# Kernel tuning notes

Measured on AMD Instinct MI355X. Metric: run time of the kernel, lower is better.

Reference implementation:

```python
import jax, jax.numpy as jnp
import numpy as np
from jax import lax

NUM_GROUPS = 16
EPS = 1e-5  # PyTorch GroupNorm default
POOL = 2
CLAMP_MIN, CLAMP_MAX = 0.0, 1.0


def setup_inputs() -> dict:
    key = jax.random.key(0)
    ks = jax.random.split(key, 6)
    B, Cin, H, W = 32, 64, 128, 128
    Cout, K = 128, 3
    return {
        "x": jax.random.normal(ks[0], (B, Cin, H, W), dtype=jnp.float32),
        "conv_w": jax.random.normal(ks[1], (Cout, Cin, K, K), dtype=jnp.float32),
        "conv_b": jax.random.normal(ks[2], (Cout,), dtype=jnp.float32),
        "gn_w": jax.random.normal(ks[3], (Cout,), dtype=jnp.float32),
        "gn_b": jax.random.normal(ks[4], (Cout,), dtype=jnp.float32),
        "scale": jax.random.normal(ks[5], (Cout, 1, 1), dtype=jnp.float32),
    }


def reference(x, conv_w, conv_b, gn_w, gn_b, scale):
    # Conv2d, stride 1, no padding (PyTorch default): [B,Cout,H-2,W-2]
    y = lax.conv_general_dilated(
        x, conv_w, window_strides=(1, 1), padding="VALID",
        dimension_numbers=("NCHW", "OIHW", "NCHW"))
    y = y + conv_b[None, :, None, None]

    # GroupNorm over (C/G, H, W) per sample and group
    B, C, H, W = y.shape
    yg = y.reshape(B, NUM_GROUPS, C // NUM_GROUPS, H, W)
    mean = jnp.mean(yg, axis=(2, 3, 4), keepdims=True)
    var = jnp.var(yg, axis=(2, 3, 4), keepdims=True)
    yn = ((yg - mean) * lax.rsqrt(var + EPS)).reshape(B, C, H, W)
    yn = yn * gn_w[None, :, None, None] + gn_b[None, :, None, None]

    # channel-wise scale (scale shape [C,1,1])
    yn = yn * scale[None, :, :, :]

    # MaxPool2d(kernel=2, stride=2)
    p = lax.reduce_window(yn, -jnp.inf, lax.max,
                          (1, 1, POOL, POOL), (1, 1, POOL, POOL), "VALID")

    # clamp
    return jnp.clip(p, CLAMP_MIN, CLAMP_MAX)
```

## Files before the change

### kernel.cpp

```cpp
#include <hip/hip_runtime.h>
#include <hip/hip_fp16.h>

#define CIN   64
#define COUT  128
#define HIN   128
#define WIN   128
#define HOUT  126
#define WOUT  126
#define HP    63
#define WP    63
#define NB    32
#define NG    16
#define EPS   1e-5f
#define KTOT  576
#define NTILE 252

#define XTROW (WIN * 64)
#define XTIMG (HIN * XTROW)

#define LROW  2176
#define LROWB 4352

typedef __attribute__((ext_vector_type(8))) _Float16 half8;
typedef __attribute__((ext_vector_type(4))) float f32x4;

#define GLOAD_LDS(gsrc, ldst)                                              \
    __builtin_amdgcn_global_load_lds(                                      \
        (const __attribute__((address_space(1))) void*)(gsrc),             \
        (__attribute__((address_space(3))) void*)(ldst), 16, 0, 0)

__global__ __launch_bounds__(256) void wprep_kernel(
    const float* __restrict__ cw, ushort* __restrict__ wt)
{
    int idx = blockIdx.x * 256 + threadIdx.x;
    if (idx >= COUT * KTOT) return;
    int co = idx / KTOT, k = idx - co * KTOT;
    int khw = k >> 6, ci = k & 63;
    float v = cw[(co * CIN + ci) * 9 + khw];
    wt[idx] = __half_as_ushort(__float2half(v));
}

__global__ __launch_bounds__(512) void xprep_kernel(
    const float* __restrict__ x, ushort* __restrict__ xt)
{
    const int tid = threadIdx.x;
    const int row = blockIdx.x & 127, b = blockIdx.x >> 7;
    const int cig = tid >> 6;
    const float* xb = x + (size_t)b * (CIN * HIN * WIN) + (size_t)row * WIN;
    ushort* ob = xt + (size_t)b * XTIMG + (size_t)row * XTROW;
#pragma unroll
    for (int ch = 0; ch < 2; ++ch) {
        int col = ch * 64 + (tid & 63);
        ushort v[8];
#pragma unroll
        for (int j = 0; j < 8; ++j)
            v[j] = __half_as_ushort(__float2half(
                xb[(size_t)(cig * 8 + j) * (HIN * WIN) + col]));
        uint4 pk;
        pk.x = (unsigned)v[0] | ((unsigned)v[1] << 16);
        pk.y = (unsigned)v[2] | ((unsigned)v[3] << 16);
        pk.z = (unsigned)v[4] | ((unsigned)v[5] << 16);
        pk.w = (unsigned)v[6] | ((unsigned)v[7] << 16);
        *(uint4*)(ob + col * 64 + ((cig ^ (col & 7)) * 8)) = pk;
    }
}

__global__ __launch_bounds__(256, 4) void conv_mfma_kernel(
    const ushort* __restrict__ xt, const ushort* __restrict__ wt,
    const float* __restrict__ cb, const float* __restrict__ gwv,
    const float* __restrict__ scv, float* __restrict__ m,
    float* __restrict__ partials)
{
    __shared__ ushort xs[4 * LROW];

    const int tid = threadIdx.x;
    const int bid = blockIdx.x;
    const int w   = (bid & 7) * 1008 + (bid >> 3);
    const int b   = w / 252;
    const int r   = w - b * 252;
    const int rp  = r >> 2;
    const int ct  = r & 3;
    const int r0x = rp * 2;

    const int l = tid & 63, wg = tid >> 6;
    const int l15 = l & 15, lhi = l >> 4;

    const ushort* xtb = xt + (size_t)b * XTIMG + (size_t)r0x * XTROW
                      + (size_t)(ct * 32) * 64;
#pragma unroll
    for (int t = 0; t < 5; ++t) {
        int idx = t * 256 + tid;
        if (idx < 1088) {
            int row = idx / 272;
            int within = idx - row * 272;
            GLOAD_LDS(xtb + (size_t)row * XTROW + within * 8, &xs[idx * 8]);
        }
    }
    __syncthreads();

    f32x4 acc[2][4];
#pragma unroll
    for (int mt = 0; mt < 2; ++mt)
#pragma unroll
        for (int nt = 0; nt < 4; ++nt)
            acc[mt][nt] = (f32x4){0.f, 0.f, 0.f, 0.f};

    const ushort* wb = wt + (size_t)(wg * 32 + l15) * KTOT + lhi * 8;
    const char* xsb = (const char*)xs;

#pragma unroll
    for (int khw = 0; khw < 9; ++khw) {
        const int kh = khw / 3, kw = khw - kh * 3;
        const int c7 = (l15 + kw) & 7;
#pragma unroll
        for (int cip = 0; cip < 2; ++cip) {
            half8 a0 = *(const half8*)(wb + khw * 64 + cip * 32);
            half8 a1 = *(const half8*)(wb + 16 * KTOT + khw * 64 + cip * 32);
            const int s = ((cip * 4 + lhi) ^ c7) * 16;
            half8 bv[4];
#pragma unroll
            for (int nt = 0; nt < 4; ++nt)
                bv[nt] = *(const half8*)(xsb + ((nt >> 1) + kh) * LROWB
                        + ((nt & 1) * 16 + kw + l15) * 128 + s);
#pragma unroll
            for (int nt = 0; nt < 4; ++nt) {
                acc[0][nt] = __builtin_amdgcn_mfma_f32_16x16x32_f16(
                    a0, bv[nt], acc[0][nt], 0, 0, 0);
                acc[1][nt] = __builtin_amdgcn_mfma_f32_16x16x32_f16(
                    a1, bv[nt], acc[1][nt], 0, 0, 0);
            }
        }
    }

#pragma unroll
    for (int mt = 0; mt < 2; ++mt) {
        float s1 = 0.f, s2 = 0.f;
#pragma unroll
        for (int r2 = 0; r2 < 4; ++r2) {
            int co = wg * 32 + mt * 16 + lhi * 4 + r2;
            float bias = cb[co];
            bool usemax = (gwv[co] * scv[co]) >= 0.f;
#pragma unroll
            for (int nc = 0; nc < 2; ++nc) {
                float v0 = acc[mt][nc][r2] + bias;
                float v1 = acc[mt][2 + nc][r2] + bias;
                int col = ct * 32 + nc * 16 + l15;
                if (col < WOUT) { s1 += v0 + v1; s2 += v0 * v0 + v1 * v1; }
                float a = usemax ? fmaxf(v0, v1) : fminf(v0, v1);
                float xo = __shfl_xor(a, 1);
                float wv = usemax ? fmaxf(a, xo) : fminf(a, xo);
                int wp = col >> 1;
                if (((l15 & 1) == 0) && wp < WP)
                    m[(((size_t)(b * COUT + co)) * HP + rp) * WP + wp] = wv;
            }
        }
#pragma unroll
        for (int d = 1; d < 16; d <<= 1) {
            s1 += __shfl_xor(s1, d);
            s2 += __shfl_xor(s2, d);
        }
        s1 += __shfl_xor(s1, 16);
        s2 += __shfl_xor(s2, 16);
        if (l15 == 0 && (lhi & 1) == 0) {
            int g = wg * 4 + mt * 2 + (lhi >> 1);
            size_t pidx = (((size_t)b * NG + g) * NTILE + (rp * 4 + ct)) * 2;
            partials[pidx + 0] = s1;
            partials[pidx + 1] = s2;
        }
    }
}

__global__ __launch_bounds__(64) void stats_kernel(
    const float* __restrict__ partials, float* __restrict__ stats)
{
    int t = blockIdx.x;
    int lane = threadIdx.x;
    float s1 = 0.f, s2 = 0.f;
    for (int j = lane; j < NTILE; j += 64) {
        s1 += partials[((size_t)t * NTILE + j) * 2 + 0];
        s2 += partials[((size_t)t * NTILE + j) * 2 + 1];
    }
#pragma unroll
    for (int d = 1; d < 64; d <<= 1) {
        s1 += __shfl_xor(s1, d);
        s2 += __shfl_xor(s2, d);
    }
    if (lane == 0) {
        const float N = 8.f * HOUT * WOUT;
        float mean = s1 / N;
        float var = s2 / N - mean * mean;
        stats[t * 2 + 0] = mean;
        stats[t * 2 + 1] = rsqrtf(var + EPS);
    }
}

__global__ __launch_bounds__(256) void final_kernel(
    const f32x4* __restrict__ m4, const float* __restrict__ stats,
    const float* __restrict__ gw, const float* __restrict__ gb,
    const float* __restrict__ sc, f32x4* __restrict__ out4)
{
    int idx = blockIdx.x * 256 + threadIdx.x;
    if (idx >= (NB * COUT * HP * WP) / 4) return;
    f32x4 v = m4[idx];
    f32x4 o;
    const int e0 = idx * 4;
#pragma unroll
    for (int j = 0; j < 4; ++j) {
        int e = e0 + j;
        int plane = e / (HP * WP);
        int c = plane & 127;
        int b = plane >> 7;
        int g = c >> 3;
        float mean = stats[(b * NG + g) * 2 + 0];
        float rstd = stats[(b * NG + g) * 2 + 1];
        float ga = rstd * gw[c] * sc[c];
        float gbb = (gb[c] - mean * rstd * gw[c]) * sc[c];
        o[j] = fminf(fmaxf(fmaf(v[j], ga, gbb), 0.f), 1.f);
    }
    out4[idx] = o;
}

extern "C" void kernel_launch(void* const* d_in, const int* in_sizes, int n_in,
                              void* d_out, int out_size, void* d_ws, size_t ws_size,
                              hipStream_t stream)
{
    const float* x  = (const float*)d_in[0];
    const float* cw = (const float*)d_in[1];
    const float* cbias = (const float*)d_in[2];
    const float* gw = (const float*)d_in[3];
    const float* gb = (const float*)d_in[4];
    const float* sc = (const float*)d_in[5];

    const size_t MSZ = (size_t)NB * COUT * HP * WP;
    float* m        = (float*)d_ws;
    float* partials = m + MSZ;
    float* stats    = partials + (size_t)NB * NG * NTILE * 2;
    ushort* wt      = (ushort*)(stats + 1024);
    ushort* xtb     = wt + (size_t)COUT * KTOT;

    hipLaunchKernelGGL(wprep_kernel, dim3((COUT * KTOT + 255) / 256), dim3(256),
                       0, stream, cw, wt);

    hipLaunchKernelGGL(xprep_kernel, dim3(NB * HIN), dim3(512), 0, stream,
                       x, xtb);

    hipLaunchKernelGGL(conv_mfma_kernel, dim3(8064), dim3(256), 0, stream,
                       xtb, wt, cbias, gw, sc, m, partials);

    hipLaunchKernelGGL(stats_kernel, dim3(NB * NG), dim3(64), 0, stream,
                       partials, stats);

    int total4 = (NB * COUT * HP * WP) / 4;
    hipLaunchKernelGGL(final_kernel, dim3((total4 + 255) / 256), dim3(256), 0, stream,
                       (const f32x4*)m, stats, gw, gb, sc, (f32x4*)d_out);
}
```

Baseline: 231.4 us.

## Widen conv tiles to 64 columns per block and store pooled intermediate as fp16

Each conv block now covers 64 output columns with 512 threads (8 waves) instead of 32 columns with 256. Overlapping halo rows are loaded into LDS once per 64 columns, which cuts the halo reload and the number of blocks. The pooled intermediate buffer is written and read as fp16 rather than fp32, halving its global traffic between the conv and final kernels. The cost is more LDS per block, which may lower occupancy, and some precision is lost on the pre-normalization pooled values.

```diff
diff --git a/kernel.cpp b/kernel.cpp
--- a/kernel.cpp
+++ b/kernel.cpp
@@ -18,10 +18,11 @@
 #define XTROW (WIN * 64)
 #define XTIMG (HIN * XTROW)
 
-#define LROW  2176
-#define LROWB 4352
+#define LROW  4224
+#define LROWB 8448
 
 typedef __attribute__((ext_vector_type(8))) _Float16 half8;
+typedef __attribute__((ext_vector_type(4))) _Float16 half4;
 typedef __attribute__((ext_vector_type(4))) float f32x4;
 
 #define GLOAD_LDS(gsrc, ldst)                                              \
@@ -65,34 +66,36 @@
     }
 }
 
-__global__ __launch_bounds__(256, 4) void conv_mfma_kernel(
+__global__ __launch_bounds__(512, 4) void conv_mfma_kernel(
     const ushort* __restrict__ xt, const ushort* __restrict__ wt,
     const float* __restrict__ cb, const float* __restrict__ gwv,
-    const float* __restrict__ scv, float* __restrict__ m,
+    const float* __restrict__ scv, ushort* __restrict__ m16,
     float* __restrict__ partials)
 {
     __shared__ ushort xs[4 * LROW];
 
     const int tid = threadIdx.x;
     const int bid = blockIdx.x;
-    const int w   = (bid & 7) * 1008 + (bid >> 3);
-    const int b   = w / 252;
-    const int r   = w - b * 252;
-    const int rp  = r >> 2;
-    const int ct  = r & 3;
-    const int r0x = rp * 2;
-
-    const int l = tid & 63, wg = tid >> 6;
+    const int w    = (bid & 7) * 504 + (bid >> 3);
+    const int b    = w / 126;
+    const int r    = w - b * 126;
+    const int rp   = r >> 1;
+    const int ct64 = r & 1;
+    const int r0x  = rp * 2;
+
+    const int l = tid & 63, wid = tid >> 6;
+    const int wg   = wid >> 1;
+    const int ch32 = wid & 1;
     const int l15 = l & 15, lhi = l >> 4;
 
     const ushort* xtb = xt + (size_t)b * XTIMG + (size_t)r0x * XTROW
-                      + (size_t)(ct * 32) * 64;
+                      + (size_t)(ct64 * 64) * 64;
 #pragma unroll
     for (int t = 0; t < 5; ++t) {
-        int idx = t * 256 + tid;
-        if (idx < 1088) {
-            int row = idx / 272;
-            int within = idx - row * 272;
+        int idx = t * 512 + tid;
+        if (idx < 2112) {
+            int row = idx / 528;
+            int within = idx - row * 528;
             GLOAD_LDS(xtb + (size_t)row * XTROW + within * 8, &xs[idx * 8]);
         }
     }
@@ -121,7 +124,7 @@
 #pragma unroll
             for (int nt = 0; nt < 4; ++nt)
                 bv[nt] = *(const half8*)(xsb + ((nt >> 1) + kh) * LROWB
-                        + ((nt & 1) * 16 + kw + l15) * 128 + s);
+                        + (ch32 * 32 + (nt & 1) * 16 + kw + l15) * 128 + s);
 #pragma unroll
             for (int nt = 0; nt < 4; ++nt) {
                 acc[0][nt] = __builtin_amdgcn_mfma_f32_16x16x32_f16(
@@ -144,14 +147,15 @@
             for (int nc = 0; nc < 2; ++nc) {
                 float v0 = acc[mt][nc][r2] + bias;
                 float v1 = acc[mt][2 + nc][r2] + bias;
-                int col = ct * 32 + nc * 16 + l15;
+                int col = ct64 * 64 + ch32 * 32 + nc * 16 + l15;
                 if (col < WOUT) { s1 += v0 + v1; s2 += v0 * v0 + v1 * v1; }
                 float a = usemax ? fmaxf(v0, v1) : fminf(v0, v1);
                 float xo = __shfl_xor(a, 1);
                 float wv = usemax ? fmaxf(a, xo) : fminf(a, xo);
                 int wp = col >> 1;
                 if (((l15 & 1) == 0) && wp < WP)
-                    m[(((size_t)(b * COUT + co)) * HP + rp) * WP + wp] = wv;
+                    ((_Float16*)m16)[(((size_t)(b * COUT + co)) * HP + rp) * WP
+                                     + wp] = (_Float16)wv;
             }
         }
 #pragma unroll
@@ -163,7 +167,8 @@
         s2 += __shfl_xor(s2, 16);
         if (l15 == 0 && (lhi & 1) == 0) {
             int g = wg * 4 + mt * 2 + (lhi >> 1);
-            size_t pidx = (((size_t)b * NG + g) * NTILE + (rp * 4 + ct)) * 2;
+            size_t pidx = (((size_t)b * NG + g) * NTILE
+                         + (rp * 4 + ct64 * 2 + ch32)) * 2;
             partials[pidx + 0] = s1;
             partials[pidx + 1] = s2;
         }
@@ -195,13 +200,13 @@
 }
 
 __global__ __launch_bounds__(256) void final_kernel(
-    const f32x4* __restrict__ m4, const float* __restrict__ stats,
+    const ushort* __restrict__ m16, const float* __restrict__ stats,
     const float* __restrict__ gw, const float* __restrict__ gb,
     const float* __restrict__ sc, f32x4* __restrict__ out4)
 {
     int idx = blockIdx.x * 256 + threadIdx.x;
     if (idx >= (NB * COUT * HP * WP) / 4) return;
-    f32x4 v = m4[idx];
+    half4 v = *(const half4*)(m16 + (size_t)idx * 4);
     f32x4 o;
     const int e0 = idx * 4;
 #pragma unroll
@@ -215,7 +220,7 @@
         float rstd = stats[(b * NG + g) * 2 + 1];
         float ga = rstd * gw[c] * sc[c];
         float gbb = (gb[c] - mean * rstd * gw[c]) * sc[c];
-        o[j] = fminf(fmaxf(fmaf(v[j], ga, gbb), 0.f), 1.f);
+        o[j] = fminf(fmaxf(fmaf((float)v[j], ga, gbb), 0.f), 1.f);
     }
     out4[idx] = o;
 }
@@ -232,8 +237,8 @@
     const float* sc = (const float*)d_in[5];
 
     const size_t MSZ = (size_t)NB * COUT * HP * WP;
-    float* m        = (float*)d_ws;
-    float* partials = m + MSZ;
+    ushort* m16     = (ushort*)d_ws;
+    float* partials = (float*)(m16 + MSZ);
     float* stats    = partials + (size_t)NB * NG * NTILE * 2;
     ushort* wt      = (ushort*)(stats + 1024);
     ushort* xtb     = wt + (size_t)COUT * KTOT;
@@ -244,13 +249,13 @@
     hipLaunchKernelGGL(xprep_kernel, dim3(NB * HIN), dim3(512), 0, stream,
                        x, xtb);
 
-    hipLaunchKernelGGL(conv_mfma_kernel, dim3(8064), dim3(256), 0, stream,
-                       xtb, wt, cbias, gw, sc, m, partials);
+    hipLaunchKernelGGL(conv_mfma_kernel, dim3(4032), dim3(512), 0, stream,
+                       xtb, wt, cbias, gw, sc, m16, partials);
 
     hipLaunchKernelGGL(stats_kernel, dim3(NB * NG), dim3(64), 0, stream,
                        partials, stats);
 
     int total4 = (NB * COUT * HP * WP) / 4;
     hipLaunchKernelGGL(final_kernel, dim3((total4 + 255) / 256), dim3(256), 0, stream,
-                       (const f32x4*)m, stats, gw, gb, sc, (f32x4*)d_out);
-}
+                       m16, stats, gw, gb, sc, (f32x4*)d_out);
+}
```

New measurement: 234.5 us. Within noise of the previous version (+1.3%).
